# Performance work log

Measured on AMD Instinct MI355X. Metric: run time of the kernel, lower is better.

## Reference

```python
import jax, jax.numpy as jnp
import numpy as np
from jax import lax

_CLIP_MIN = 1e-06
_CLIP_MAX = 1.0
_POS_ALPHA = 0.0005
NUM_CLASSES = 21
RADIUS = 3
HALF_D = RADIUS * RADIUS
POOL = 3
PAD = POOL // 2
IGNORE = 255
LAM = 0.5  # loss_weight_lambda, lambda_way=1


def _max_pool(x):
    # NCHW max pool, kernel=stride=3, padding=1
    return lax.reduce_window(x, -jnp.inf, lax.max,
                             (1, 1, POOL, POOL), (1, 1, POOL, POOL),
                             ((0, 0), (0, 0), (PAD, PAD), (PAD, PAD)))


def _get_pairs(x):
    # stack radius*radius shifted crops -> [N, C, r^2, nh, nw]
    h, w = x.shape[2], x.shape[3]
    nh, nw = h - RADIUS + 1, w - RADIUS + 1
    crops = [x[:, :, y:y + nh, xo:xo + nw] for y in range(RADIUS) for xo in range(RADIUS)]
    return jnp.stack(crops, axis=2)


def _log_det_by_cholesky(m):
    chol = jnp.linalg.cholesky(m)
    return 2.0 * jnp.sum(jnp.log(jnp.diagonal(chol, axis1=-2, axis2=-1) + 1e-08), axis=-1)


def _rmi_lower_bound(labels_4d, probs_4d):
    la = _max_pool(labels_4d)
    pr = _max_pool(probs_4d)
    n, c = la.shape[0], la.shape[1]
    la_v = _get_pairs(la).reshape(n, c, HALF_D, -1)   # [N,C,d,L]
    pr_v = _get_pairs(pr).reshape(n, c, HALF_D, -1)
    la_v = la_v - jnp.mean(la_v, axis=3, keepdims=True)
    pr_v = pr_v - jnp.mean(pr_v, axis=3, keepdims=True)
    la_cov = jnp.einsum('ncdl,ncel->ncde', la_v, la_v)
    pr_cov = jnp.einsum('ncdl,ncel->ncde', pr_v, pr_v)
    eye = jnp.eye(HALF_D, dtype=la_cov.dtype)
    pr_cov_inv = jnp.linalg.inv(pr_cov + eye * _POS_ALPHA)
    la_pr_cov = jnp.einsum('ncdl,ncel->ncde', la_v, pr_v)
    appro_var = la_cov - jnp.einsum('ncde,ncef,ncgf->ncdg', la_pr_cov, pr_cov_inv, la_pr_cov)
    rmi_now = 0.5 * _log_det_by_cholesky(appro_var + eye * _POS_ALPHA)  # [N,C]
    rmi_per_class = jnp.mean(rmi_now.reshape(-1, NUM_CLASSES), axis=0) / float(HALF_D)
    return jnp.sum(rmi_per_class)


def setup_inputs() -> dict:
    key = jax.random.key(0)
    k1, k2 = jax.random.split(key)
    score = jax.random.normal(k1, (4, NUM_CLASSES, 512, 512), dtype=jnp.float32)
    target = jax.random.randint(k2, (4, 512, 512), 0, NUM_CLASSES, dtype=jnp.int64)
    return {"score": score, "target": target}


def reference(score, target):
    # cross entropy with ignore_index=255, mean reduction
    logp = jax.nn.log_softmax(score, axis=1)                      # [N,C,H,W]
    valid_ce = (target != IGNORE)
    safe_t = jnp.where(valid_ce, target, 0)
    nll = -jnp.take_along_axis(logp, safe_t[:, None].astype(jnp.int32), axis=1)[:, 0]
    normal_loss = jnp.sum(jnp.where(valid_ce, nll, 0.0)) / jnp.sum(valid_ce.astype(jnp.float32))

    # valid one-hot labels and masked sigmoid probs
    mask = (target < NUM_CLASSES)                                 # [N,H,W]
    maskf = mask.astype(jnp.float32)
    onehot = jax.nn.one_hot((target * mask).astype(jnp.int32), NUM_CLASSES, dtype=jnp.float32)
    onehot = onehot * maskf[..., None]                            # [N,H,W,C]
    onehot = jnp.transpose(onehot, (0, 3, 1, 2))                  # [N,C,H,W]
    probs = jnp.clip(jax.nn.sigmoid(score) * maskf[:, None], _CLIP_MIN, _CLIP_MAX)

    rmi_loss = _rmi_lower_bound(onehot, probs)
    return LAM * normal_loss + rmi_loss * (1.0 - LAM)
```

## Files before the change

kernel.cpp:

```cpp
#include <hip/hip_runtime.h>
#include <cfloat>
#include <cmath>

#define DEVINL __device__ __forceinline__

constexpr int N_ = 4, C_ = 21, H_ = 512, W_ = 512;
constexpr int P_ = 171;
constexpr int Q_ = 169;
constexpr int NC_ = N_ * C_;
constexpr int HW_ = H_ * W_;
constexpr int PP_ = P_ * P_;
constexpr int NCOV_ = 189;
constexpr float EPS_ = 5e-4f;

DEVINL constexpr int tstart(int d) { return d * 9 - d * (d - 1) / 2; }

DEVINL float wave_sum(float v) {
#pragma unroll
    for (int o = 32; o > 0; o >>= 1) v += __shfl_down(v, o, 64);
    return v;
}

__global__ __launch_bounds__(256) void k_fused(const float* __restrict__ score,
                                               const int* __restrict__ target,
                                               float* __restrict__ pr,
                                               float* __restrict__ la,
                                               float* __restrict__ cov_ce) {
    int gid = blockIdx.x * 256 + threadIdx.x;
    float nll = 0.f, cnt = 0.f;
    if (gid < N_ * PP_) {
        int j = gid % P_;
        int i = (gid / P_) % P_;
        int n = gid / PP_;
        float prmax[C_];
#pragma unroll
        for (int c = 0; c < C_; ++c) prmax[c] = -FLT_MAX;
        unsigned lamask = 0;
        const float* sbase = score + (size_t)n * C_ * HW_;
        const int* tbase = target + (size_t)n * HW_;
        int h0 = 3 * i - 1, w0 = 3 * j - 1;
#pragma unroll
        for (int dy = 0; dy < 3; ++dy) {
            int h = h0 + dy;
            if (h < 0 || h >= H_) continue;
#pragma unroll
            for (int dx = 0; dx < 3; ++dx) {
                int w = w0 + dx;
                if (w < 0 || w >= W_) continue;
                int t = tbase[h * W_ + w];
                const float* sp = sbase + h * W_ + w;
                float s[C_];
#pragma unroll
                for (int c = 0; c < C_; ++c) s[c] = sp[(size_t)c * HW_];
                float m = s[0];
#pragma unroll
                for (int c = 1; c < C_; ++c) m = fmaxf(m, s[c]);
                float se = 0.f;
#pragma unroll
                for (int c = 0; c < C_; ++c) se += __expf(s[c] - m);
                float lse = m + __logf(se);
                if (t != 255) {
                    int tc = (t >= 0 && t < C_) ? t : 0;
                    nll += (lse - s[tc]);
                    cnt += 1.f;
                }
                bool maskv = (t >= 0 && t < C_);
                if (maskv) lamask |= (1u << t);
                float mf = maskv ? 1.f : 0.f;
#pragma unroll
                for (int c = 0; c < C_; ++c) {
                    float p = mf * __builtin_amdgcn_rcpf(1.f + __expf(-s[c]));
                    p = fminf(fmaxf(p, 1e-6f), 1.f);
                    prmax[c] = fmaxf(prmax[c], p);
                }
            }
        }
        size_t ob = (size_t)n * C_ * PP_ + (size_t)i * P_ + j;
#pragma unroll
        for (int c = 0; c < C_; ++c) {
            pr[ob + (size_t)c * PP_] = prmax[c];
            la[ob + (size_t)c * PP_] = ((lamask >> c) & 1u) ? 1.f : 0.f;
        }
    }
    nll = wave_sum(nll);
    cnt = wave_sum(cnt);
    if ((threadIdx.x & 63) == 0) {
        atomicAdd(&cov_ce[NC_ * NCOV_ + 0], nll);
        atomicAdd(&cov_ce[NC_ * NCOV_ + 1], cnt);
    }
}

__global__ __launch_bounds__(256, 2) void k_cov(const float* __restrict__ la,
                                                const float* __restrict__ pr,
                                                float* __restrict__ cov) {
    int nc = blockIdx.x;
    int chunk = blockIdx.y;
    const float* A = la + (size_t)nc * PP_;
    const float* B = pr + (size_t)nc * PP_;
    constexpr int RC = 29;
    int r0 = chunk * RC;
    int rend = r0 + RC;
    if (rend > Q_) rend = Q_;
    int npts = (rend - r0) * Q_;

    float sA[9], sB[9], SAA[45], SBB[45], SAB[81];
#pragma unroll
    for (int k = 0; k < 9; ++k) { sA[k] = 0.f; sB[k] = 0.f; }
#pragma unroll
    for (int k = 0; k < 45; ++k) { SAA[k] = 0.f; SBB[k] = 0.f; }
#pragma unroll
    for (int k = 0; k < 81; ++k) SAB[k] = 0.f;

    for (int idx = threadIdx.x; idx < npts; idx += 256) {
        int lr = idx / Q_;
        int col = idx - lr * Q_;
        int row = r0 + lr;
        const float* ap = A + row * P_ + col;
        const float* bp = B + row * P_ + col;
        float a[9], b[9];
#pragma unroll
        for (int dy = 0; dy < 3; ++dy)
#pragma unroll
            for (int dx = 0; dx < 3; ++dx) {
                a[dy * 3 + dx] = ap[dy * P_ + dx];
                b[dy * 3 + dx] = bp[dy * P_ + dx];
            }
#pragma unroll
        for (int d = 0; d < 9; ++d) { sA[d] += a[d]; sB[d] += b[d]; }
        {
            int k = 0;
#pragma unroll
            for (int d = 0; d < 9; ++d)
#pragma unroll
                for (int e = d; e < 9; ++e) {
                    SAA[k] += a[d] * a[e];
                    SBB[k] += b[d] * b[e];
                    ++k;
                }
        }
#pragma unroll
        for (int d = 0; d < 9; ++d)
#pragma unroll
            for (int e = 0; e < 9; ++e) SAB[d * 9 + e] += a[d] * b[e];
    }

    __shared__ float red[4][NCOV_];
    int lane = threadIdx.x & 63;
    int wv = threadIdx.x >> 6;
#pragma unroll
    for (int d = 0; d < 9; ++d) { float v = wave_sum(sA[d]); if (lane == 0) red[wv][d] = v; }
#pragma unroll
    for (int d = 0; d < 9; ++d) { float v = wave_sum(sB[d]); if (lane == 0) red[wv][9 + d] = v; }
#pragma unroll
    for (int k = 0; k < 45; ++k) { float v = wave_sum(SAA[k]); if (lane == 0) red[wv][18 + k] = v; }
#pragma unroll
    for (int k = 0; k < 45; ++k) { float v = wave_sum(SBB[k]); if (lane == 0) red[wv][63 + k] = v; }
#pragma unroll
    for (int k = 0; k < 81; ++k) { float v = wave_sum(SAB[k]); if (lane == 0) red[wv][108 + k] = v; }
    __syncthreads();
    for (int k = threadIdx.x; k < NCOV_; k += 256) {
        float v = red[0][k] + red[1][k] + red[2][k] + red[3][k];
        atomicAdd(&cov[nc * NCOV_ + k], v);
    }
}

__global__ __launch_bounds__(128) void k_final(const float* __restrict__ cov,
                                               float* __restrict__ out) {
    __shared__ float red[128];
    int t = threadIdx.x;
    float my = 0.f;
    if (t < NC_) {
        const float* S = cov + t * NCOV_;
        const float Lf = (float)(Q_ * Q_);
        float sA[9], sB[9];
#pragma unroll
        for (int d = 0; d < 9; ++d) { sA[d] = S[d]; sB[d] = S[9 + d]; }
        float laC[45], M[45], Cm[81];
        {
            int k = 0;
#pragma unroll
            for (int d = 0; d < 9; ++d)
#pragma unroll
                for (int e = d; e < 9; ++e) {
                    laC[k] = S[18 + k] - sA[d] * sA[e] / Lf;
                    M[k] = S[63 + k] - sB[d] * sB[e] / Lf + (d == e ? EPS_ : 0.f);
                    ++k;
                }
#pragma unroll
            for (int d = 0; d < 9; ++d)
#pragma unroll
                for (int e = 0; e < 9; ++e)
                    Cm[d * 9 + e] = S[108 + d * 9 + e] - sA[d] * sB[e] / Lf;
        }
#pragma unroll
        for (int j = 0; j < 9; ++j) {
            float s = M[tstart(j)];
#pragma unroll
            for (int k = 0; k < j; ++k) { float l = M[tstart(k) + (j - k)]; s -= l * l; }
            float dj = sqrtf(fmaxf(s, 1e-30f));
            M[tstart(j)] = dj;
            float inv = 1.f / dj;
#pragma unroll
            for (int i = j + 1; i < 9; ++i) {
                float s2 = M[tstart(j) + (i - j)];
#pragma unroll
                for (int k = 0; k < j; ++k)
                    s2 -= M[tstart(k) + (i - k)] * M[tstart(k) + (j - k)];
                M[tstart(j) + (i - j)] = s2 * inv;
            }
        }
#pragma unroll
        for (int p = 0; p < 9; ++p) {
#pragma unroll
            for (int i = 0; i < 9; ++i) {
                float s = Cm[p * 9 + i];
#pragma unroll
                for (int k = 0; k < i; ++k)
                    s -= M[tstart(k) + (i - k)] * Cm[p * 9 + k];
                Cm[p * 9 + i] = s / M[tstart(i)];
            }
        }
#pragma unroll
        for (int d = 0; d < 9; ++d)
#pragma unroll
            for (int e = d; e < 9; ++e) {
                float s = 0.f;
#pragma unroll
                for (int i = 0; i < 9; ++i) s += Cm[d * 9 + i] * Cm[e * 9 + i];
                laC[tstart(d) + (e - d)] -= s;
                if (d == e) laC[tstart(d)] += EPS_;
            }
        float rmi = 0.f;
#pragma unroll
        for (int j = 0; j < 9; ++j) {
            float s = laC[tstart(j)];
#pragma unroll
            for (int k = 0; k < j; ++k) { float l = laC[tstart(k) + (j - k)]; s -= l * l; }
            float dj = sqrtf(fmaxf(s, 0.f));
            laC[tstart(j)] = dj;
            float inv = 1.f / fmaxf(dj, 1e-30f);
#pragma unroll
            for (int i = j + 1; i < 9; ++i) {
                float s2 = laC[tstart(j) + (i - j)];
#pragma unroll
                for (int k = 0; k < j; ++k)
                    s2 -= laC[tstart(k) + (i - k)] * laC[tstart(k) + (j - k)];
                laC[tstart(j) + (i - j)] = s2 * inv;
            }
            rmi += __logf(dj + 1e-8f);
        }
        my = rmi;
    }
    red[t] = my;
    __syncthreads();
#pragma unroll
    for (int o = 64; o > 0; o >>= 1) {
        if (t < o) red[t] += red[t + o];
        __syncthreads();
    }
    if (t == 0) {
        float rmi_total = red[0] / 36.f;
        float ce = cov[NC_ * NCOV_ + 0] / cov[NC_ * NCOV_ + 1];
        out[0] = 0.5f * ce + 0.5f * rmi_total;
    }
}

extern "C" void kernel_launch(void* const* d_in, const int* in_sizes, int n_in,
                              void* d_out, int out_size, void* d_ws, size_t ws_size,
                              hipStream_t stream) {
    const float* score = (const float*)d_in[0];
    const int* target = (const int*)d_in[1];
    float* pr = (float*)d_ws;
    float* la = pr + (size_t)NC_ * PP_;
    float* cov = la + (size_t)NC_ * PP_;
    hipMemsetAsync(cov, 0, (size_t)(NC_ * NCOV_ + 2) * sizeof(float), stream);

    int nthreads = N_ * PP_;
    k_fused<<<dim3((nthreads + 255) / 256), dim3(256), 0, stream>>>(score, target, pr, la, cov);
    dim3 g2(NC_, 6);
    k_cov<<<g2, dim3(256), 0, stream>>>(la, pr, cov);
    k_final<<<dim3(1), dim3(128), 0, stream>>>(cov, (float*)d_out);
}
```

Baseline: 261.3 us.

## Restructure pooling kernel into row-per-block separable max pool through shared memory

Each block now handles one pooled output row. Threads walk contiguous image columns, so global loads of score and target are coalesced instead of strided by three. Each thread reduces its three source rows into a per-column channel max kept in shared memory, and a second pass reduces columns into pooled outputs. The clip is moved after the max, which is equivalent because clipping is monotonic. The cost is about 45KB of shared memory per block and a block barrier, which can limit occupancy.

```diff
diff --git a/kernel.cpp b/kernel.cpp
--- a/kernel.cpp
+++ b/kernel.cpp
@@ -26,62 +26,74 @@
                                                float* __restrict__ pr,
                                                float* __restrict__ la,
                                                float* __restrict__ cov_ce) {
-    int gid = blockIdx.x * 256 + threadIdx.x;
+    __shared__ float sP[C_][W_];
+    __shared__ unsigned sM[W_];
+    int bid = blockIdx.x;
+    int i = bid % P_;
+    int n = bid / P_;
+    const float* sbase = score + (size_t)n * C_ * HW_;
+    const int* tbase = target + (size_t)n * HW_;
+    int h0 = 3 * i - 1;
+    int hlo = h0 < 0 ? 0 : h0;
+    int hhi = h0 + 2;
+
     float nll = 0.f, cnt = 0.f;
-    if (gid < N_ * PP_) {
-        int j = gid % P_;
-        int i = (gid / P_) % P_;
-        int n = gid / PP_;
-        float prmax[C_];
-#pragma unroll
-        for (int c = 0; c < C_; ++c) prmax[c] = -FLT_MAX;
-        unsigned lamask = 0;
-        const float* sbase = score + (size_t)n * C_ * HW_;
-        const int* tbase = target + (size_t)n * HW_;
-        int h0 = 3 * i - 1, w0 = 3 * j - 1;
-#pragma unroll
-        for (int dy = 0; dy < 3; ++dy) {
-            int h = h0 + dy;
-            if (h < 0 || h >= H_) continue;
-#pragma unroll
-            for (int dx = 0; dx < 3; ++dx) {
-                int w = w0 + dx;
-                if (w < 0 || w >= W_) continue;
-                int t = tbase[h * W_ + w];
-                const float* sp = sbase + h * W_ + w;
-                float s[C_];
-#pragma unroll
-                for (int c = 0; c < C_; ++c) s[c] = sp[(size_t)c * HW_];
-                float m = s[0];
-#pragma unroll
-                for (int c = 1; c < C_; ++c) m = fmaxf(m, s[c]);
-                float se = 0.f;
-#pragma unroll
-                for (int c = 0; c < C_; ++c) se += __expf(s[c] - m);
-                float lse = m + __logf(se);
-                if (t != 255) {
-                    int tc = (t >= 0 && t < C_) ? t : 0;
-                    nll += (lse - s[tc]);
-                    cnt += 1.f;
-                }
-                bool maskv = (t >= 0 && t < C_);
-                if (maskv) lamask |= (1u << t);
-                float mf = maskv ? 1.f : 0.f;
-#pragma unroll
-                for (int c = 0; c < C_; ++c) {
-                    float p = mf * __builtin_amdgcn_rcpf(1.f + __expf(-s[c]));
-                    p = fminf(fmaxf(p, 1e-6f), 1.f);
-                    prmax[c] = fmaxf(prmax[c], p);
-                }
-            }
-        }
-        size_t ob = (size_t)n * C_ * PP_ + (size_t)i * P_ + j;
-#pragma unroll
-        for (int c = 0; c < C_; ++c) {
-            pr[ob + (size_t)c * PP_] = prmax[c];
-            la[ob + (size_t)c * PP_] = ((lamask >> c) & 1u) ? 1.f : 0.f;
-        }
-    }
+    for (int w = threadIdx.x; w < W_; w += 256) {
+        float vmax[C_];
+#pragma unroll
+        for (int c = 0; c < C_; ++c) vmax[c] = 0.f;
+        unsigned lm = 0;
+        for (int h = hlo; h <= hhi; ++h) {
+            const float* sp = sbase + (size_t)h * W_ + w;
+            int t = tbase[h * W_ + w];
+            float s[C_];
+#pragma unroll
+            for (int c = 0; c < C_; ++c) s[c] = sp[(size_t)c * HW_];
+            float m = s[0];
+#pragma unroll
+            for (int c = 1; c < C_; ++c) m = fmaxf(m, s[c]);
+            float se = 0.f;
+#pragma unroll
+            for (int c = 0; c < C_; ++c) se += __expf(s[c] - m);
+            float lse = m + __logf(se);
+            if (t != 255) {
+                int tc = (t >= 0 && t < C_) ? t : 0;
+                nll += (lse - s[tc]);
+                cnt += 1.f;
+            }
+            bool mv = (t >= 0 && t < C_);
+            if (mv) lm |= (1u << t);
+            float mf = mv ? 1.f : 0.f;
+#pragma unroll
+            for (int c = 0; c < C_; ++c) {
+                float p = mf * __builtin_amdgcn_rcpf(1.f + __expf(-s[c]));
+                vmax[c] = fmaxf(vmax[c], p);
+            }
+        }
+#pragma unroll
+        for (int c = 0; c < C_; ++c) sP[c][w] = vmax[c];
+        sM[w] = lm;
+    }
+    __syncthreads();
+
+    size_t ob = (size_t)n * C_ * PP_ + (size_t)i * P_;
+    for (int item = threadIdx.x; item < C_ * P_; item += 256) {
+        int c = item / P_;
+        int j = item - c * P_;
+        int w0 = 3 * j - 1;
+        int wl = w0 < 0 ? 0 : w0;
+        int wh = w0 + 2 > W_ - 1 ? W_ - 1 : w0 + 2;
+        float m = 0.f;
+        unsigned bits = 0;
+        for (int w = wl; w <= wh; ++w) {
+            m = fmaxf(m, sP[c][w]);
+            bits |= sM[w];
+        }
+        m = fminf(fmaxf(m, 1e-6f), 1.f);
+        pr[ob + (size_t)c * PP_ + j] = m;
+        la[ob + (size_t)c * PP_ + j] = ((bits >> c) & 1u) ? 1.f : 0.f;
+    }
+
     nll = wave_sum(nll);
     cnt = wave_sum(cnt);
     if ((threadIdx.x & 63) == 0) {
@@ -275,8 +287,7 @@
     float* cov = la + (size_t)NC_ * PP_;
     hipMemsetAsync(cov, 0, (size_t)(NC_ * NCOV_ + 2) * sizeof(float), stream);
 
-    int nthreads = N_ * PP_;
-    k_fused<<<dim3((nthreads + 255) / 256), dim3(256), 0, stream>>>(score, target, pr, la, cov);
+    k_fused<<<dim3(N_ * P_), dim3(256), 0, stream>>>(score, target, pr, la, cov);
     dim3 g2(NC_, 6);
     k_cov<<<g2, dim3(256), 0, stream>>>(la, pr, cov);
     k_final<<<dim3(1), dim3(128), 0, stream>>>(cov, (float*)d_out);
```

Measured after the change: 282.3 us. 1.08x slower.
